# Kernel tuning notes

Hardware: AMD Instinct MI355X
Metric: run time of the kernel (lower is better)

## Reference

```python
import jax, jax.numpy as jnp
import numpy as np
import math

D_MODEL = 1024
N_HEADS = 16
RANK = 16
SCALE = 16.0
T_LEN = 2048
BSZ = 2


def setup_inputs() -> dict:
    key = jax.random.key(0)
    ks = jax.random.split(key, 12)
    d, r = D_MODEL, RANK
    inp = {
        "query": jax.random.normal(ks[0], (T_LEN, BSZ, d), dtype=jnp.float32),
        "key": jax.random.normal(ks[1], (T_LEN, BSZ, d), dtype=jnp.float32),
        "value": jax.random.normal(ks[2], (T_LEN, BSZ, d), dtype=jnp.float32),
        "need_weights": 0,
        "attn_mask": 0,
        "in_proj_weight": jax.random.normal(ks[3], (3 * d, d), dtype=jnp.float32) * 0.02,
        "in_proj_bias": jax.random.normal(ks[4], (3 * d,), dtype=jnp.float32) * 0.02,
        "out_w": jax.random.normal(ks[5], (d, d), dtype=jnp.float32) * 0.02,
        "out_b": jax.random.normal(ks[6], (d,), dtype=jnp.float32) * 0.02,
        "k_a": jax.random.normal(ks[7], (r, d), dtype=jnp.float32) * 0.02,
        "k_b": jax.random.normal(ks[8], (r, d), dtype=jnp.float32) * 0.02,
        "v_a": jax.random.normal(ks[9], (r, d), dtype=jnp.float32) * 0.02,
        "v_b": jax.random.normal(ks[10], (r, d), dtype=jnp.float32) * 0.02,
    }
    return inp


def reference(query, key, value, need_weights, attn_mask,
              in_proj_weight, in_proj_bias, out_w, out_b,
              k_a, k_b, v_a, v_b):
    # NOTE: original module computes q,k,v all from `query` (self-attention);
    # `key`, `value`, `need_weights`, `attn_mask` are unused in the math.
    T, B, d = query.shape
    H = N_HEADS
    hd = d // H
    qkv = query @ in_proj_weight.T + in_proj_bias  # (T, B, 3d)
    q, k, v = jnp.split(qkv, 3, axis=-1)
    s = SCALE / RANK
    # LoRA low-rank updates on K and V (computed from query)
    k = k + s * ((query @ k_a.T) @ k_b)
    v = v + s * ((query @ v_a.T) @ v_b)
    # split heads: (T, B, H, hd)
    qh = q.reshape(T, B, H, hd)
    kh = k.reshape(T, B, H, hd)
    vh = v.reshape(T, B, H, hd)
    scale = 1.0 / math.sqrt(hd)
    scores = jnp.einsum('tbhd,sbhd->bhts', qh * scale, kh)  # (B, H, T, T)
    attn = jax.nn.softmax(scores, axis=-1)
    out = jnp.einsum('bhts,sbhd->tbhd', attn, vh).reshape(T, B, d)
    out = out @ out_w.T + out_b
    return out
```

## Files before the change

### kernel.cpp

```cpp
#include <hip/hip_runtime.h>
#include <stdint.h>

#define DEVI __device__ __forceinline__

typedef unsigned short u16;
typedef __attribute__((ext_vector_type(4))) float f32x4;
typedef __attribute__((ext_vector_type(16))) float f32x16;
typedef __attribute__((ext_vector_type(8))) short bf16x8;
typedef __attribute__((ext_vector_type(2))) unsigned int u32x2;

constexpr int T_LEN = 2048;
constexpr int BSZ   = 2;
constexpr int DM    = 1024;
constexpr int NH    = 16;
constexpr int HD    = 64;
constexpr int MROWS = T_LEN * BSZ;
constexpr float LORA_S = 16.0f / 16.0f;
constexpr float QSCALE = 0.125f * 1.4426950408889634f;

DEVI u16 f2bf(float x) {
  union { float f; uint32_t u; } v; v.f = x;
  uint32_t r = (v.u + 0x7FFFu + ((v.u >> 16) & 1u)) >> 16;
  return (u16)r;
}

DEVI uint32_t pk2bf(float a, float b) {
  return (uint32_t)f2bf(a) | ((uint32_t)f2bf(b) << 16);
}

DEVI uint32_t e2r(float x) {
  union { float f; uint32_t u; } v;
  v.f = __builtin_amdgcn_exp2f(x);
  return v.u;
}

DEVI void gload_lds16(const void* g, void* l) {
  __builtin_amdgcn_global_load_lds(
      (const __attribute__((address_space(1))) void*)g,
      (__attribute__((address_space(3))) void*)l, 16, 0, 0);
}

DEVI f32x4 mfma16(bf16x8 a, bf16x8 b, f32x4 c) {
  return __builtin_amdgcn_mfma_f32_16x16x32_bf16(a, b, c, 0, 0, 0);
}
DEVI f32x16 mfma32(bf16x8 a, bf16x8 b, f32x16 c) {
  return __builtin_amdgcn_mfma_f32_32x32x16_bf16(a, b, c, 0, 0, 0);
}

DEVI int kvswz(int rc, int l) { return rc * 128 + ((l ^ (rc & 15)) << 3); }

#define WAITBAR(N)                                        \
  do {                                                    \
    asm volatile("s_waitcnt vmcnt(" #N ")" ::: "memory"); \
    __builtin_amdgcn_sched_barrier(0);                    \
    __builtin_amdgcn_s_barrier();                         \
    __builtin_amdgcn_sched_barrier(0);                    \
  } while (0)

#define BARO()                                            \
  do {                                                    \
    __builtin_amdgcn_sched_barrier(0);                    \
    __builtin_amdgcn_s_barrier();                         \
    __builtin_amdgcn_sched_barrier(0);                    \
  } while (0)

__global__ void prep_kernel(const float* __restrict__ query,
                            const float* __restrict__ W,
                            const float* __restrict__ ka, const float* __restrict__ kb,
                            const float* __restrict__ va, const float* __restrict__ vb,
                            const float* __restrict__ ow,
                            u16* __restrict__ Wm, u16* __restrict__ Wo,
                            u16* __restrict__ Aq) {
  const int W3 = 3 * DM * DM;
  const int WO = DM * DM;
  const int AQ = MROWS * DM;
  const int total = W3 + WO + AQ;
  for (int idx = blockIdx.x * blockDim.x + threadIdx.x; idx < total;
       idx += gridDim.x * blockDim.x) {
    if (idx < W3) {
      const int n = idx >> 10, k = idx & 1023;
      float w = W[idx];
      if (n >= 2 * DM) {
        const int n2 = n - 2 * DM;
        float a = 0.f;
#pragma unroll
        for (int r = 0; r < 16; ++r) a += va[r * DM + k] * vb[r * DM + n2];
        w += LORA_S * a;
      } else if (n >= DM) {
        const int n2 = n - DM;
        float a = 0.f;
#pragma unroll
        for (int r = 0; r < 16; ++r) a += ka[r * DM + k] * kb[r * DM + n2];
        w += LORA_S * a;
      }
      Wm[idx] = f2bf(w);
    } else if (idx < W3 + WO) {
      const int i = idx - W3;
      Wo[i] = f2bf(ow[i]);
    } else {
      const int i = idx - W3 - WO;
      Aq[i] = f2bf(query[i]);
    }
  }
}

__global__ __launch_bounds__(512) void gemm256_qkv(
    const u16* __restrict__ A, const u16* __restrict__ Bt,
    const float* __restrict__ bias,
    u16* __restrict__ Qb, u16* __restrict__ Kb, u16* __restrict__ Vt) {
  constexpr int K = DM;
  constexpr int BK = 32;
  __shared__ alignas(16) u16 SM[4][2][128 * 64];
  const int tid = threadIdx.x;
  const int wv = tid >> 6, ln = tid & 63;
  const int l16 = ln & 15, lhi = ln >> 4;
  const int wm = wv >> 2, wn = wv & 3;
  const int row0 = blockIdx.x * 256, col0 = blockIdx.y * 256;

  f32x4 acc[8][4];
#pragma unroll
  for (int m = 0; m < 8; ++m)
#pragma unroll
    for (int n = 0; n < 4; ++n) acc[m][n] = f32x4{0.f, 0.f, 0.f, 0.f};

  const int rr0 = wv * 16 + (ln >> 3);
  const int sl_ = ln & 7;
  const int v0 = sl_ ^ (rr0 & 7);
  const int lrow0 = rr0 + 128 * (v0 >> 2);
  const int c0 = (v0 & 3) * 8;

  const u16* pa = A + (size_t)(row0 + lrow0) * K + c0;
  const u16* pb = Bt + (size_t)(col0 + lrow0) * K + c0;

  auto stagep = [&](int buf) {
    gload_lds16(pa, &SM[buf][0][(wv * 16) * 64]);
    gload_lds16(pa + (size_t)8 * K, &SM[buf][0][(wv * 16 + 8) * 64]);
    gload_lds16(pb, &SM[buf][1][(wv * 16) * 64]);
    gload_lds16(pb + (size_t)8 * K, &SM[buf][1][(wv * 16 + 8) * 64]);
    pa += BK; pb += BK;
  };

  auto compute = [&](int buf) {
    const u16* Al = SM[buf][0];
    const u16* Bl = SM[buf][1];
    bf16x8 af[8], bfr[4];
#pragma unroll
    for (int m = 0; m < 8; ++m) {
      const int rr = m * 16 + l16;
      const int sl = (lhi | (wm << 2)) ^ (rr & 7);
      af[m] = *(const bf16x8*)&Al[rr * 64 + sl * 8];
    }
#pragma unroll
    for (int n = 0; n < 4; ++n) {
      const int c = wn * 64 + n * 16 + l16;
      const int rr = c & 127;
      const int sl = (lhi | ((c >> 7) << 2)) ^ (rr & 7);
      bfr[n] = *(const bf16x8*)&Bl[rr * 64 + sl * 8];
    }
    __builtin_amdgcn_s_setprio(1);
#pragma unroll
    for (int m = 0; m < 8; ++m)
#pragma unroll
      for (int n = 0; n < 4; ++n) acc[m][n] = mfma16(af[m], bfr[n], acc[m][n]);
    __builtin_amdgcn_s_setprio(0);
  };

  constexpr int NS = K / BK;
  stagep(0); stagep(1); stagep(2);

  for (int t4 = 0; t4 < NS - 4; t4 += 4) {
    WAITBAR(8); compute(0); stagep(3);
    WAITBAR(8); compute(1); stagep(0);
    WAITBAR(8); compute(2); stagep(1);
    WAITBAR(8); compute(3); stagep(2);
  }
  WAITBAR(8); compute(0); stagep(3);
  WAITBAR(8); compute(1);
  WAITBAR(4); compute(2);
  WAITBAR(0); compute(3);

  if (col0 >= 2 * DM) {
    u16* Cl = (u16*)SM;
    __syncthreads();
#pragma unroll
    for (int m = 0; m < 8; ++m)
#pragma unroll
      for (int n = 0; n < 4; ++n) {
        const int lc = wn * 64 + n * 16 + l16;
        const float bc = bias[col0 + lc];
#pragma unroll
        for (int r = 0; r < 4; ++r) {
          const int rl = wm * 128 + m * 16 + lhi * 4 + r;
          const int tl = rl >> 1, bb = rl & 1;
          Cl[lc * 256 + bb * 128 + (((tl >> 3) ^ (lc & 7)) << 3) + (tl & 7)] =
              f2bf(acc[m][n][r] + bc);
        }
      }
    __syncthreads();
    const int h0 = (col0 - 2 * DM) >> 6;
    const int t0 = row0 >> 1;
#pragma unroll
    for (int i = 0; i < 16; ++i) {
      const int cid = i * 512 + tid;
      const int lc = cid >> 5, bb = (cid >> 4) & 1, tc = cid & 15;
      bf16x8 ch = *(const bf16x8*)&Cl[lc * 256 + bb * 128 + ((tc ^ (lc & 7)) << 3)];
      const int h = h0 + (lc >> 6), dd = lc & 63;
      *(bf16x8*)&Vt[(((size_t)(bb * NH + h)) * HD + dd) * T_LEN + t0 + tc * 8] = ch;
    }
    return;
  }

#pragma unroll
  for (int m = 0; m < 8; ++m) {
#pragma unroll
    for (int n = 0; n < 4; ++n) {
      const int col = col0 + wn * 64 + n * 16 + l16;
      const float bc = bias[col];
#pragma unroll
      for (int r = 0; r < 4; ++r) {
        const int row = row0 + wm * 128 + m * 16 + lhi * 4 + r;
        const float v = acc[m][n][r] + bc;
        const int t = row >> 1, b = row & 1;
        if (col < DM) {
          const int h = col >> 6, dd = col & 63;
          Qb[(((size_t)(b * NH + h)) * T_LEN + t) * HD + dd] = f2bf(v * QSCALE);
        } else {
          const int c2 = col - DM, h = c2 >> 6, dd = c2 & 63;
          Kb[(((size_t)(b * NH + h)) * T_LEN + t) * HD + dd] = f2bf(v);
        }
      }
    }
  }
}

template <int EPIL>
__global__ __launch_bounds__(256) void gemm_bt(
    const u16* __restrict__ A, const u16* __restrict__ Bt,
    const float* __restrict__ bias, float* __restrict__ Cf,
    u16* __restrict__ Qb, u16* __restrict__ Kb, u16* __restrict__ Vt,
    int M, int N, int K) {
  constexpr int BM = 128, BN = 128, BK = 32;
  __shared__ alignas(16) u16 SM[4][2][4096];
  const int tid = threadIdx.x;
  const int wv = tid >> 6, ln = tid & 63;
  const int l16 = ln & 15, lhi = ln >> 4;
  const int row0 = blockIdx.x * BM, col0 = blockIdx.y * BN;
  const int wr = (wv >> 1) * 64, wc = (wv & 1) * 64;

  f32x4 acc[4][4];
#pragma unroll
  for (int i = 0; i < 4; ++i)
#pragma unroll
    for (int j2 = 0; j2 < 4; ++j2) acc[i][j2] = f32x4{0.f, 0.f, 0.f, 0.f};

  const int lrA = wv * 16 + (ln >> 3);
  const int lrB = lrA + 8;
  const int s_ = ln & 7;
  const int la = s_ ^ (lrA & 7), lb = s_ ^ (lrB & 7);
  const int ra = lrA + 64 * (la >> 2), ca = (la & 3) * 8;
  const int rb = lrB + 64 * (lb >> 2), cb = (lb & 3) * 8;

  const u16* pa0 = A + (size_t)(row0 + ra) * K + ca;
  const u16* pa1 = A + (size_t)(row0 + rb) * K + cb;
  const u16* pb0 = Bt + (size_t)(col0 + ra) * K + ca;
  const u16* pb1 = Bt + (size_t)(col0 + rb) * K + cb;

  auto stagep = [&](int buf) {
    gload_lds16(pa0, &SM[buf][0][(wv * 16) * 64]);
    gload_lds16(pa1, &SM[buf][0][(wv * 16 + 8) * 64]);
    gload_lds16(pb0, &SM[buf][1][(wv * 16) * 64]);
    gload_lds16(pb1, &SM[buf][1][(wv * 16 + 8) * 64]);
    pa0 += BK; pa1 += BK; pb0 += BK; pb1 += BK;
  };

  auto compute = [&](int buf) {
    const u16* Al = SM[buf][0];
    const u16* Bl = SM[buf][1];
    bf16x8 af[4], bfr[4];
#pragma unroll
    for (int m = 0; m < 4; ++m) {
      const int r = wr + m * 16 + l16, lr = r & 63;
      const int sl = (lhi | ((r >> 6) << 2)) ^ (lr & 7);
      af[m] = *(const bf16x8*)&Al[lr * 64 + sl * 8];
    }
#pragma unroll
    for (int n = 0; n < 4; ++n) {
      const int r = wc + n * 16 + l16, lr = r & 63;
      const int sl = (lhi | ((r >> 6) << 2)) ^ (lr & 7);
      bfr[n] = *(const bf16x8*)&Bl[lr * 64 + sl * 8];
    }
#pragma unroll
    for (int m = 0; m < 4; ++m)
#pragma unroll
      for (int n = 0; n < 4; ++n) acc[m][n] = mfma16(af[m], bfr[n], acc[m][n]);
  };

  const int NS = K / BK;
  stagep(0); stagep(1); stagep(2);

  for (int t4 = 0; t4 < NS - 4; t4 += 4) {
    WAITBAR(8); compute(0); stagep(3);
    WAITBAR(8); compute(1); stagep(0);
    WAITBAR(8); compute(2); stagep(1);
    WAITBAR(8); compute(3); stagep(2);
  }
  WAITBAR(8); compute(0); stagep(3);
  WAITBAR(8); compute(1);
  WAITBAR(4); compute(2);
  WAITBAR(0); compute(3);

#pragma unroll
  for (int m = 0; m < 4; ++m) {
#pragma unroll
    for (int n = 0; n < 4; ++n) {
      const int col = col0 + wc + n * 16 + l16;
      const float bc = bias[col];
#pragma unroll
      for (int r = 0; r < 4; ++r) {
        const int row = row0 + wr + m * 16 + lhi * 4 + r;
        const float v = acc[m][n][r] + bc;
        Cf[(size_t)row * N + col] = v;
      }
    }
  }
}

__global__ __launch_bounds__(256) void attn_kernel(const u16* __restrict__ Qb,
                                                   const u16* __restrict__ Kb,
                                                   const u16* __restrict__ Vt,
                                                   u16* __restrict__ Ob) {
  constexpr int KBLK = 64;
  __shared__ alignas(16) u16 KV[4][2][32 * 128];

  const int tid = threadIdx.x;
  const int wv = tid >> 6, ln = tid & 63;
  const int l32 = ln & 31, hi = ln >> 5;

  const int bid = blockIdx.x;
  const int lb = (bid & 7) * 64 + (bid >> 3);
  const int bh = lb >> 4;
  const int b = bh >> 4, h = bh & 15;
  const int q0 = (lb & 15) * 128 + wv * 32;

  const u16* Qh = Qb + (size_t)bh * T_LEN * HD;
  const u16* Kh = Kb + (size_t)bh * T_LEN * HD;
  const u16* Vh = Vt + (size_t)bh * HD * T_LEN;

  bf16x8 qf[4];
#pragma unroll
  for (int kd = 0; kd < 4; ++kd)
    qf[kd] = *(const bf16x8*)&Qh[(size_t)(q0 + l32) * HD + kd * 16 + hi * 8];

  bf16x8 ones;
#pragma unroll
  for (int i = 0; i < 8; ++i) ones[i] = (short)0x3F80;

  f32x16 ot[2] = {f32x16{}, f32x16{}};
  f32x16 lacc = f32x16{};

  const int g_row = ln >> 4;
  const int g_s   = ln & 15;
  const int j0 = wv * 2, j1 = wv * 2 + 1;
  const int row0r = 4 * j0 + g_row, row1r = 4 * j1 + g_row;
  const int l0 = g_s ^ (row0r & 15), l1 = g_s ^ (row1r & 15);
  const int lr0 = row0r + 32 * (l0 >> 3), lr1 = row1r + 32 * (l1 >> 3);
  const int c80 = (l0 & 7) * 8, c81 = (l1 & 7) * 8;

  const u16* ks0 = Kh + (size_t)lr0 * HD + c80;
  const u16* ks1 = Kh + (size_t)lr1 * HD + c81;
  const u16* vs0 = Vh + (size_t)lr0 * T_LEN + c80;
  const u16* vs1 = Vh + (size_t)lr1 * T_LEN + c81;

  auto stagep = [&](int buf) {
    gload_lds16(ks0, &KV[buf][0][j0 * 512]);
    gload_lds16(ks1, &KV[buf][0][j1 * 512]);
    gload_lds16(vs0, &KV[buf][1][j0 * 512]);
    gload_lds16(vs1, &KV[buf][1][j1 * 512]);
    ks0 += KBLK * HD; ks1 += KBLK * HD; vs0 += KBLK; vs1 += KBLK;
  };

  auto compute = [&](int buf) {
    const u16* Kl = KV[buf][0];
    const u16* Vl = KV[buf][1];
    f32x16 st[2] = {f32x16{}, f32x16{}};
    __builtin_amdgcn_s_setprio(1);
#pragma unroll
    for (int kd = 0; kd < 4; ++kd) {
      bf16x8 k0 = *(const bf16x8*)&Kl[kvswz(l32, kd * 2 + hi)];
      bf16x8 k1 = *(const bf16x8*)&Kl[kvswz(l32, 8 + kd * 2 + hi)];
      st[0] = mfma32(k0, qf[kd], st[0]);
      st[1] = mfma32(k1, qf[kd], st[1]);
    }
    __builtin_amdgcn_s_setprio(0);
    uint32_t c[2][8];
#pragma unroll
    for (int mk = 0; mk < 2; ++mk)
#pragma unroll
      for (int d = 0; d < 8; ++d)
        c[mk][d] = __builtin_amdgcn_perm(e2r(st[mk][2 * d + 1]),
                                         e2r(st[mk][2 * d]), 0x07060302u);
    __builtin_amdgcn_s_setprio(1);
#pragma unroll
    for (int ksl = 0; ksl < 4; ++ksl) {
      const int mk = ksl >> 1, s2 = ksl & 1;
      uint32_t a0 = c[mk][4 * s2 + 0], b0 = c[mk][4 * s2 + 2];
      uint32_t a1 = c[mk][4 * s2 + 1], b1 = c[mk][4 * s2 + 3];
      u32x2 r0 = __builtin_amdgcn_permlane32_swap(a0, b0, false, false);
      u32x2 r1 = __builtin_amdgcn_permlane32_swap(a1, b1, false, false);
      union { bf16x8 v; uint32_t u[4]; } pu;
      pu.u[0] = r0[0]; pu.u[1] = r1[0]; pu.u[2] = r0[1]; pu.u[3] = r1[1];
      bf16x8 vf0 = *(const bf16x8*)&Vl[kvswz(l32, ksl * 2 + hi)];
      bf16x8 vf1 = *(const bf16x8*)&Vl[kvswz(l32, 8 + ksl * 2 + hi)];
      ot[0] = mfma32(vf0, pu.v, ot[0]);
      ot[1] = mfma32(vf1, pu.v, ot[1]);
      lacc = mfma32(ones, pu.v, lacc);
    }
    __builtin_amdgcn_s_setprio(0);
  };

  stagep(0); stagep(1); stagep(2); stagep(3);

  for (int it7 = 0; it7 < 7; ++it7) {
    WAITBAR(8); compute(0); compute(1); BARO(); stagep(0); stagep(1);
    WAITBAR(8); compute(2); compute(3); BARO(); stagep(2); stagep(3);
  }
  WAITBAR(8); compute(0); compute(1);
  WAITBAR(0); compute(2); compute(3);

  const float inv = 1.0f / lacc[0];
  const size_t rowbase = ((size_t)(q0 + l32) * BSZ + b) * DM + h * HD;
#pragma unroll
  for (int dt = 0; dt < 2; ++dt) {
#pragma unroll
    for (int g = 0; g < 4; ++g) {
      const float v0 = ot[dt][4 * g + 0] * inv;
      const float v1 = ot[dt][4 * g + 1] * inv;
      const float v2 = ot[dt][4 * g + 2] * inv;
      const float v3 = ot[dt][4 * g + 3] * inv;
      u32x2 w; w[0] = pk2bf(v0, v1); w[1] = pk2bf(v2, v3);
      const int dim = dt * 32 + 8 * g + 4 * hi;
      *(u32x2*)&Ob[rowbase + dim] = w;
    }
  }
}

extern "C" void kernel_launch(void* const* d_in, const int* in_sizes, int n_in,
                              void* d_out, int out_size, void* d_ws, size_t ws_size,
                              hipStream_t stream) {
  const float* query = (const float*)d_in[0];
  const float* W     = (const float*)d_in[5];
  const float* bias  = (const float*)d_in[6];
  const float* ow    = (const float*)d_in[7];
  const float* ob    = (const float*)d_in[8];
  const float* ka    = (const float*)d_in[9];
  const float* kb    = (const float*)d_in[10];
  const float* va    = (const float*)d_in[11];
  const float* vb    = (const float*)d_in[12];

  char* ws = (char*)d_ws;
  u16* Wm = (u16*)ws; ws += (size_t)3 * DM * DM * 2;
  u16* Wo = (u16*)ws; ws += (size_t)DM * DM * 2;
  u16* Aq = (u16*)ws; ws += (size_t)MROWS * DM * 2;
  u16* Qb = (u16*)ws; ws += (size_t)BSZ * NH * T_LEN * HD * 2;
  u16* Kb = (u16*)ws; ws += (size_t)BSZ * NH * T_LEN * HD * 2;
  u16* Vt = (u16*)ws; ws += (size_t)BSZ * NH * T_LEN * HD * 2;
  u16* Ob = (u16*)ws; ws += (size_t)MROWS * DM * 2;

  prep_kernel<<<2048, 256, 0, stream>>>(query, W, ka, kb, va, vb, ow, Wm, Wo, Aq);

  gemm256_qkv<<<dim3(MROWS / 256, (3 * DM) / 256), 512, 0, stream>>>(
      Aq, Wm, bias, Qb, Kb, Vt);

  attn_kernel<<<512, 256, 0, stream>>>(Qb, Kb, Vt, Ob);

  gemm_bt<1><<<dim3(MROWS / 128, DM / 128), 256, 0, stream>>>(
      Ob, Wo, ob, (float*)d_out, nullptr, nullptr, nullptr, MROWS, DM, DM);
}
```

Measured before the change: 110.9 us.

## Retile QKV GEMM to 128x256 blocks with 256 threads and 3-stage pipeline

The fused QKV projection GEMM now uses 128-row by 256-column tiles with four waves instead of 256x256 tiles with eight waves. The LDS pipeline shrinks from four stages to three, and load and fragment indexing is reworked to match. This doubles the block count so the grid better fills the GPU's compute units, at the cost of less operand reuse per block. The output GEMM is also de-templated as cleanup.

```diff
diff --git a/kernel.cpp b/kernel.cpp
--- a/kernel.cpp
+++ b/kernel.cpp
@@ -104,18 +104,17 @@
   }
 }
 
-__global__ __launch_bounds__(512) void gemm256_qkv(
+__global__ __launch_bounds__(256) void gemm_qkv(
     const u16* __restrict__ A, const u16* __restrict__ Bt,
     const float* __restrict__ bias,
     u16* __restrict__ Qb, u16* __restrict__ Kb, u16* __restrict__ Vt) {
   constexpr int K = DM;
   constexpr int BK = 32;
-  __shared__ alignas(16) u16 SM[4][2][128 * 64];
+  __shared__ alignas(16) u16 SM[3][12288];
   const int tid = threadIdx.x;
   const int wv = tid >> 6, ln = tid & 63;
   const int l16 = ln & 15, lhi = ln >> 4;
-  const int wm = wv >> 2, wn = wv & 3;
-  const int row0 = blockIdx.x * 256, col0 = blockIdx.y * 256;
+  const int row0 = blockIdx.x * 128, col0 = blockIdx.y * 256;
 
   f32x4 acc[8][4];
 #pragma unroll
@@ -123,37 +122,45 @@
 #pragma unroll
     for (int n = 0; n < 4; ++n) acc[m][n] = f32x4{0.f, 0.f, 0.f, 0.f};
 
-  const int rr0 = wv * 16 + (ln >> 3);
-  const int sl_ = ln & 7;
-  const int v0 = sl_ ^ (rr0 & 7);
-  const int lrow0 = rr0 + 128 * (v0 >> 2);
-  const int c0 = (v0 & 3) * 8;
-
-  const u16* pa = A + (size_t)(row0 + lrow0) * K + c0;
-  const u16* pb = Bt + (size_t)(col0 + lrow0) * K + c0;
+  const int s_ = ln & 7;
+  const int lrA0 = wv * 16 + (ln >> 3);
+  const int lrA1 = lrA0 + 8;
+  const int vA0 = s_ ^ (lrA0 & 7), vA1 = s_ ^ (lrA1 & 7);
+  const u16* pa0 = A + (size_t)(row0 + lrA0 + 64 * (vA0 >> 2)) * K + (vA0 & 3) * 8;
+  const u16* pa1 = A + (size_t)(row0 + lrA1 + 64 * (vA1 >> 2)) * K + (vA1 & 3) * 8;
+  const int rb0 = wv * 32 + (ln >> 3), rb1 = rb0 + 8, rb2 = rb0 + 16, rb3 = rb0 + 24;
+  const int vB0 = s_ ^ (rb0 & 7), vB1 = s_ ^ (rb1 & 7);
+  const int vB2 = s_ ^ (rb2 & 7), vB3 = s_ ^ (rb3 & 7);
+  const u16* pb0 = Bt + (size_t)(col0 + rb0 + 128 * (vB0 >> 2)) * K + (vB0 & 3) * 8;
+  const u16* pb1 = Bt + (size_t)(col0 + rb1 + 128 * (vB1 >> 2)) * K + (vB1 & 3) * 8;
+  const u16* pb2 = Bt + (size_t)(col0 + rb2 + 128 * (vB2 >> 2)) * K + (vB2 & 3) * 8;
+  const u16* pb3 = Bt + (size_t)(col0 + rb3 + 128 * (vB3 >> 2)) * K + (vB3 & 3) * 8;
 
   auto stagep = [&](int buf) {
-    gload_lds16(pa, &SM[buf][0][(wv * 16) * 64]);
-    gload_lds16(pa + (size_t)8 * K, &SM[buf][0][(wv * 16 + 8) * 64]);
-    gload_lds16(pb, &SM[buf][1][(wv * 16) * 64]);
-    gload_lds16(pb + (size_t)8 * K, &SM[buf][1][(wv * 16 + 8) * 64]);
-    pa += BK; pb += BK;
+    u16* Al = SM[buf];
+    u16* Bl = SM[buf] + 4096;
+    gload_lds16(pa0, &Al[(wv * 16) * 64]);
+    gload_lds16(pa1, &Al[(wv * 16 + 8) * 64]);
+    gload_lds16(pb0, &Bl[(wv * 32) * 64]);
+    gload_lds16(pb1, &Bl[(wv * 32 + 8) * 64]);
+    gload_lds16(pb2, &Bl[(wv * 32 + 16) * 64]);
+    gload_lds16(pb3, &Bl[(wv * 32 + 24) * 64]);
+    pa0 += BK; pa1 += BK; pb0 += BK; pb1 += BK; pb2 += BK; pb3 += BK;
   };
 
   auto compute = [&](int buf) {
-    const u16* Al = SM[buf][0];
-    const u16* Bl = SM[buf][1];
+    const u16* Al = SM[buf];
+    const u16* Bl = SM[buf] + 4096;
     bf16x8 af[8], bfr[4];
 #pragma unroll
     for (int m = 0; m < 8; ++m) {
-      const int rr = m * 16 + l16;
-      const int sl = (lhi | (wm << 2)) ^ (rr & 7);
-      af[m] = *(const bf16x8*)&Al[rr * 64 + sl * 8];
+      const int r = m * 16 + l16, lr = r & 63;
+      const int sl = (lhi | ((r >> 6) << 2)) ^ (lr & 7);
+      af[m] = *(const bf16x8*)&Al[lr * 64 + sl * 8];
     }
 #pragma unroll
     for (int n = 0; n < 4; ++n) {
-      const int c = wn * 64 + n * 16 + l16;
-      const int rr = c & 127;
+      const int c = wv * 64 + n * 16 + l16, rr = c & 127;
       const int sl = (lhi | ((c >> 7) << 2)) ^ (rr & 7);
       bfr[n] = *(const bf16x8*)&Bl[rr * 64 + sl * 8];
     }
@@ -166,18 +173,15 @@
   };
 
   constexpr int NS = K / BK;
-  stagep(0); stagep(1); stagep(2);
-
-  for (int t4 = 0; t4 < NS - 4; t4 += 4) {
-    WAITBAR(8); compute(0); stagep(3);
-    WAITBAR(8); compute(1); stagep(0);
-    WAITBAR(8); compute(2); stagep(1);
-    WAITBAR(8); compute(3); stagep(2);
-  }
-  WAITBAR(8); compute(0); stagep(3);
-  WAITBAR(8); compute(1);
-  WAITBAR(4); compute(2);
-  WAITBAR(0); compute(3);
+  stagep(0); stagep(1);
+
+  for (int t3 = 0; t3 < NS - 2; t3 += 3) {
+    WAITBAR(6); compute(0); stagep(2);
+    WAITBAR(6); compute(1); stagep(0);
+    WAITBAR(6); compute(2); stagep(1);
+  }
+  WAITBAR(6); compute(0);
+  WAITBAR(0); compute(1);
 
   if (col0 >= 2 * DM) {
     u16* Cl = (u16*)SM;
@@ -186,13 +190,13 @@
     for (int m = 0; m < 8; ++m)
 #pragma unroll
       for (int n = 0; n < 4; ++n) {
-        const int lc = wn * 64 + n * 16 + l16;
+        const int lc = wv * 64 + n * 16 + l16;
         const float bc = bias[col0 + lc];
 #pragma unroll
         for (int r = 0; r < 4; ++r) {
-          const int rl = wm * 128 + m * 16 + lhi * 4 + r;
+          const int rl = m * 16 + lhi * 4 + r;
           const int tl = rl >> 1, bb = rl & 1;
-          Cl[lc * 256 + bb * 128 + (((tl >> 3) ^ (lc & 7)) << 3) + (tl & 7)] =
+          Cl[lc * 128 + bb * 64 + (((tl >> 3) ^ (lc & 7)) << 3) + (tl & 7)] =
               f2bf(acc[m][n][r] + bc);
         }
       }
@@ -201,9 +205,9 @@
     const int t0 = row0 >> 1;
 #pragma unroll
     for (int i = 0; i < 16; ++i) {
-      const int cid = i * 512 + tid;
-      const int lc = cid >> 5, bb = (cid >> 4) & 1, tc = cid & 15;
-      bf16x8 ch = *(const bf16x8*)&Cl[lc * 256 + bb * 128 + ((tc ^ (lc & 7)) << 3)];
+      const int cid = i * 256 + tid;
+      const int lc = cid >> 4, bb = (cid >> 3) & 1, tc = cid & 7;
+      bf16x8 ch = *(const bf16x8*)&Cl[lc * 128 + bb * 64 + ((tc ^ (lc & 7)) << 3)];
       const int h = h0 + (lc >> 6), dd = lc & 63;
       *(bf16x8*)&Vt[(((size_t)(bb * NH + h)) * HD + dd) * T_LEN + t0 + tc * 8] = ch;
     }
@@ -214,11 +218,11 @@
   for (int m = 0; m < 8; ++m) {
 #pragma unroll
     for (int n = 0; n < 4; ++n) {
-      const int col = col0 + wn * 64 + n * 16 + l16;
+      const int col = col0 + wv * 64 + n * 16 + l16;
       const float bc = bias[col];
 #pragma unroll
       for (int r = 0; r < 4; ++r) {
-        const int row = row0 + wm * 128 + m * 16 + lhi * 4 + r;
+        const int row = row0 + m * 16 + lhi * 4 + r;
         const float v = acc[m][n][r] + bc;
         const int t = row >> 1, b = row & 1;
         if (col < DM) {
@@ -233,12 +237,9 @@
   }
 }
 
-template <int EPIL>
-__global__ __launch_bounds__(256) void gemm_bt(
+__global__ __launch_bounds__(256) void gemm_out(
     const u16* __restrict__ A, const u16* __restrict__ Bt,
-    const float* __restrict__ bias, float* __restrict__ Cf,
-    u16* __restrict__ Qb, u16* __restrict__ Kb, u16* __restrict__ Vt,
-    int M, int N, int K) {
+    const float* __restrict__ bias, float* __restrict__ Cf, int M, int N, int K) {
   constexpr int BM = 128, BN = 128, BK = 32;
   __shared__ alignas(16) u16 SM[4][2][4096];
   const int tid = threadIdx.x;
@@ -318,8 +319,7 @@
 #pragma unroll
       for (int r = 0; r < 4; ++r) {
         const int row = row0 + wr + m * 16 + lhi * 4 + r;
-        const float v = acc[m][n][r] + bc;
-        Cf[(size_t)row * N + col] = v;
+        Cf[(size_t)row * N + col] = acc[m][n][r] + bc;
       }
     }
   }
@@ -468,11 +468,11 @@
 
   prep_kernel<<<2048, 256, 0, stream>>>(query, W, ka, kb, va, vb, ow, Wm, Wo, Aq);
 
-  gemm256_qkv<<<dim3(MROWS / 256, (3 * DM) / 256), 512, 0, stream>>>(
+  gemm_qkv<<<dim3(MROWS / 128, (3 * DM) / 256), 256, 0, stream>>>(
       Aq, Wm, bias, Qb, Kb, Vt);
 
   attn_kernel<<<512, 256, 0, stream>>>(Qb, Kb, Vt, Ob);
 
-  gemm_bt<1><<<dim3(MROWS / 128, DM / 128), 256, 0, stream>>>(
-      Ob, Wo, ob, (float*)d_out, nullptr, nullptr, nullptr, MROWS, DM, DM);
-}
+  gemm_out<<<dim3(MROWS / 128, DM / 128), 256, 0, stream>>>(
+      Ob, Wo, ob, (float*)d_out, MROWS, DM, DM);
+}
```

Result: slower. 123.3 us (+11.1%).
